# Performance work log

Measured on AMD Instinct MI355X. Metric: run time of the kernel, lower is better.

The kernel has to match this reference:

```python
import jax, jax.numpy as jnp
import numpy as np

V, B, NP, NJ = 5, 32, 20, 17
NB = 16
ND = 128
POSE_MIN_DEPTH, POSE_MAX_DEPTH = 2000.0, 8000.0
POSE_SIGMA = 100.0
KS = 11
HIDDEN_ROUGH, HIDDEN = 1024, 1024
BONES = np.array([[0,1],[0,2],[1,3],[2,4],[5,6],[5,7],[7,9],[6,8],[8,10],[5,11],[6,12],[11,12],[11,13],[13,15],[12,14],[14,16]], dtype=np.int32)


def setup_inputs() -> dict:
    key = jax.random.key(0)
    ks = jax.random.split(key, 12)
    wh = jnp.array([1920.0, 1080.0], jnp.float32)
    kpts = jax.random.uniform(ks[0], (V, B, NP, NJ, 2), jnp.float32) * wh
    pose_vis = jnp.ones((V, B, NP), jnp.float32)
    joint_vis = (jax.random.uniform(ks[1], (V, B, NP, NJ)) > 0.15).astype(jnp.float32)
    gt_pose_depths = jax.random.uniform(ks[2], (B, NP), jnp.float32, 2000.0, 8000.0)
    gt_joint_depths = jax.random.uniform(ks[3], (B, NP, NJ), jnp.float32, -100.0, 100.0)
    angles = np.linspace(-0.3, 0.3, V)
    Rs = np.stack([np.array([[np.cos(a), 0.0, np.sin(a)], [0.0, 1.0, 0.0], [-np.sin(a), 0.0, np.cos(a)]], dtype=np.float32) for a in angles])
    cam_R = jnp.broadcast_to(jnp.asarray(Rs)[:, None], (V, B, 3, 3))
    tvec = np.zeros((V, 3), np.float32); tvec[:, 0] = np.linspace(-500.0, 500.0, V)
    cam_T = jnp.broadcast_to(jnp.asarray(tvec)[:, None], (V, B, 3))
    cam_f = jnp.full((V, B, 2), 1400.0, jnp.float32)
    cam_c = jnp.broadcast_to(jnp.array([960.0, 540.0], jnp.float32), (V, B, 2))
    image_wh = jnp.broadcast_to(jnp.array([1920.0, 1080.0], jnp.float32), (V, B, 2))
    num_persons = jax.random.randint(ks[4], (V, B), 10, NP + 1, jnp.int32)
    Wr1 = jax.random.normal(ks[5], (HIDDEN_ROUGH, NJ * 2)) * 0.02
    br1 = jnp.zeros((HIDDEN_ROUGH,), jnp.float32)
    Wr2 = jax.random.normal(ks[6], (NJ, HIDDEN_ROUGH)) * 0.02
    br2 = jnp.zeros((NJ,), jnp.float32)
    Wc1 = jax.random.normal(ks[7], (HIDDEN, NJ + NB, 3)) * 0.02
    bc1 = jnp.zeros((HIDDEN,), jnp.float32)
    Wc2 = jax.random.normal(ks[8], (1, HIDDEN, 3)) * 0.02
    bc2 = jnp.zeros((1,), jnp.float32)
    bones = jnp.asarray(BONES)
    return dict(kpts=kpts, pose_vis=pose_vis, joint_vis=joint_vis, gt_pose_depths=gt_pose_depths, gt_joint_depths=gt_joint_depths, cam_R=cam_R, cam_T=cam_T, cam_f=cam_f, cam_c=cam_c, image_wh=image_wh, num_persons=num_persons, Wr1=Wr1, br1=br1, Wr2=Wr2, br2=br2, Wc1=Wc1, bc1=bc1, Wc2=Wc2, bc2=bc2, bones=bones)


def _bone_len(p, bones):
    # p: [B, Np, Nj, D, 2] -> [B, Np, Nb, D]
    a = p[:, :, bones[:, 0]]
    b = p[:, :, bones[:, 1]]
    return jnp.sqrt(jnp.sum((a - b) ** 2, -1) + 1e-12)


def _conv1d(x, w, b):
    # x [N,C,L], w [O,I,3]
    y = jax.lax.conv_general_dilated(x, w, (1,), 'SAME', dimension_numbers=('NCH', 'OIH', 'NCH'))
    return y + b[None, :, None]


def _forward(kpts, joint_vis, cam_R, cam_T, cam_f, cam_c, image_wh, num_persons, Wr1, br1, Wr2, br2, Wc1, bc1, Wc2, bc2, bones):
    V_, B_, NP_, NJ_, _ = kpts.shape
    labels = jnp.arange(ND, dtype=jnp.float32) / (ND - 1) * (POSE_MAX_DEPTH - POSE_MIN_DEPTH) + POSE_MIN_DEPTH
    kt = kpts[0]  # target-view 2D poses [B,Np,Nj,2]
    # faithful to original indexing quirk: normalize all batches by batch-0 image size
    kn = kt / image_wh[0, 0][None, None, None, :]
    x = kn.reshape(B_ * NP_, NJ_ * 2)
    h = jax.nn.relu(x @ Wr1.T + br1)
    rough = (h @ Wr2.T + br2).reshape(B_, NP_, NJ_) * 1000.0
    rough = jax.lax.stop_gradient(rough)  # .detach() in original
    depths = labels[None, None, None, :] + rough[..., None]  # [B,Np,Nj,D]
    # back-project target 2D poses at every depth hypothesis
    R0, T0, f0, c0 = cam_R[0], cam_T[0], cam_f[0], cam_c[0]
    uvn = (kt - c0[:, None, None, :]) / f0[:, None, None, :]
    xy = uvn[..., None, :] * depths[..., None]
    cam_pts = jnp.concatenate([xy, depths[..., None]], -1)
    p3d = jnp.einsum('bji,bpkdj->bpkdi', R0, cam_pts) + T0[:, None, None, None, :]  # world [B,Np,Nj,D,3]

    scores = scores2 = boundings = boundings2 = None
    for rv in range(1, V_):
        Rr, Tr, fr, cr = cam_R[rv], cam_T[rv], cam_f[rv], cam_c[rv]
        xc = jnp.einsum('bij,bpkdj->bpkdi', Rr, p3d - Tr[:, None, None, None, :])
        p2t = xc[..., :2] / (xc[..., 2:3] + 1e-8) * fr[:, None, None, None, :] + cr[:, None, None, None, :]
        pr = kpts[rv]         # [B,Npr,Nj,2]
        vr = joint_vis[rv]    # [B,Npr,Nj]
        # pairwise dist over (target-person, ref-person) per joint/depth
        d = jnp.sum((p2t[:, :, None] - pr[:, None, :, :, None, :]) ** 2, -1)  # [B,Npt,Npr,Nj,D]
        w = vr[:, None, :, :, None]
        pdist = jnp.sum(d * w, 3) / (jnp.sum(w, 3) + 1e-8)  # [B,Npt,Npr,D]
        valid = jnp.arange(NP_)[None, None, :, None] < num_persons[rv][:, None, None, None]
        pdist = jnp.where(valid, pdist, 1e5)
        mm = jnp.argmin(pdist, 2)  # [B,Npt,D] nearest ref pose
        bidx = jnp.arange(B_)[:, None, None]
        matched = jnp.transpose(pr[bidx, mm], (0, 1, 3, 2, 4))  # [B,Npt,Nj,D,2]
        mvis = jnp.transpose(vr[bidx, mm], (0, 1, 3, 2))        # [B,Npt,Nj,D]
        mdist = jnp.sum((p2t - matched) ** 2, -1)
        score = jnp.exp(-jnp.sqrt(mdist + 1e-12) / POSE_SIGMA)  # panoptic branch
        score_bl = jnp.exp(-jnp.abs(_bone_len(matched, bones) - _bone_len(p2t, bones)) / 5.0)
        wimg = image_wh[rv][:, None, None, None, 0]
        himg = image_wh[rv][:, None, None, None, 1]
        inb = ((p2t[..., 0] >= 0) & (p2t[..., 1] >= 0) & (p2t[..., 0] <= wimg - 1) & (p2t[..., 1] <= himg - 1)).astype(score.dtype)
        bounding = inb * mvis
        bounding2 = jnp.broadcast_to(mvis[:, :, :1, :], score_bl.shape)
        if scores is None:
            scores, scores2 = score * bounding, score_bl * bounding2
            boundings, boundings2 = bounding, bounding2
        else:
            scores = scores + score * bounding
            scores2 = scores2 + score_bl * bounding2
            boundings = boundings + bounding
            boundings2 = boundings2 + bounding2
    psv = (scores / (boundings + 1e-8)).reshape(B_ * NP_, NJ_, ND)
    psv2 = (scores2 / (boundings2 + 1e-8)).reshape(B_ * NP_, NB, ND)
    xin = jnp.concatenate([psv, psv2], 1)  # [BN, Nj+Nb, D]
    hc = jax.nn.relu(_conv1d(xin, Wc1, bc1))
    logits = _conv1d(hc, Wc2, bc2)[:, 0, :]  # [BN, D]
    vol = jax.nn.softmax(logits, -1)
    # soft-argmax restricted to a window around the argmax
    pos = jnp.arange(ND, dtype=vol.dtype)
    idx = jnp.argmax(vol, -1)
    mask = (jnp.abs(pos[None, :] - idx[:, None].astype(vol.dtype)) <= KS // 2).astype(vol.dtype)
    mv = vol * mask
    mv = mv / (jnp.sum(mv, -1, keepdims=True) + 1e-8)
    pred_idx = jnp.sum(mv * pos, -1).reshape(B_, NP_)
    return pred_idx / (ND - 1) * (POSE_MAX_DEPTH - POSE_MIN_DEPTH) + POSE_MIN_DEPTH


def reference(kpts, pose_vis, joint_vis, gt_pose_depths, gt_joint_depths, cam_R, cam_T, cam_f, cam_c, image_wh, num_persons, Wr1, br1, Wr2, br2, Wc1, bc1, Wc2, bc2, bones):
    return _forward(kpts, joint_vis, cam_R, cam_T, cam_f, cam_c, image_wh, num_persons, Wr1, br1, Wr2, br2, Wc1, bc1, Wc2, bc2, bones)
```

## Files before the change

kernel.cpp:

```cpp
#include <hip/hip_runtime.h>
#include <math.h>

#define VV  5
#define BB  32
#define NPP 20
#define NJJ 17
#define NBB 16
#define NDD 128
#define HID 1024
#define KPITCH 128
#define KSTEPS 7
#define PRP 36
#define VRP 20
#define NCH 34
#define A_T_ELEMS (32 * KSTEPS * 64 * 8)
#define EPI_ELEMS (32 * 4 * 64 * 16)

typedef __attribute__((ext_vector_type(8))) short short8;
typedef __attribute__((ext_vector_type(16))) float float16;

static constexpr int BONE_A[NBB] = {0,0,1,2,5,5,7,6,8,5,6,11,11,13,12,14};
static constexpr int BONE_B[NBB] = {1,2,3,4,6,7,9,8,10,11,12,12,13,15,14,16};

__device__ __forceinline__ float warp_red_sum(float v) {
#pragma unroll
  for (int off = 32; off >= 1; off >>= 1) v += __shfl_xor(v, off, 64);
  return v;
}

__global__ __launch_bounds__(256) void prep_kernel(
    const float* __restrict__ Wc1, const float* __restrict__ Wc2,
    const float* __restrict__ bc1,
    unsigned short* __restrict__ A_hi, unsigned short* __restrict__ A_lo,
    float* __restrict__ epi) {
  int gidx = blockIdx.x * 256 + threadIdx.x;
  if (gidx < A_T_ELEMS) {
    int e = gidx & 7;
    int l = (gidx >> 3) & 63;
    int rest = gidx >> 9;
    int ks = rest % 7;
    int ot = rest / 7;
    int o = ot * 32 + (l & 31);
    int kk = ks * 16 + (l >> 5) * 8 + e;
    float x = (kk < 99) ? Wc1[o * 99 + kk] : 0.0f;
    unsigned int u = __float_as_uint(x);
    unsigned short hi = (unsigned short)(u >> 16);
    float xh = __uint_as_float((u >> 16) << 16);
    unsigned short lo = (unsigned short)(__float_as_uint(x - xh) >> 16);
    A_hi[gidx] = hi;
    A_lo[gidx] = lo;
  } else {
    int idx2 = gidx - A_T_ELEMS;
    if (idx2 < EPI_ELEMS) {
      int c = idx2 & 15;
      int l = (idx2 >> 4) & 63;
      int rb = (idx2 >> 10) & 3;
      int ot = idx2 >> 12;
      int base = ot * 32 + 4 * (l >> 5) + 8 * rb;
      epi[idx2] = (c < 12) ? Wc2[base * 3 + c] : bc1[base + (c - 12)];
    }
  }
}

__global__ __launch_bounds__(512, 4) void pose_front_kernel(
    const float* __restrict__ kpts, const float* __restrict__ joint_vis,
    const float* __restrict__ cam_R, const float* __restrict__ cam_T,
    const float* __restrict__ cam_f, const float* __restrict__ cam_c,
    const float* __restrict__ image_wh, const int* __restrict__ num_persons,
    const float* __restrict__ Wr1, const float* __restrict__ br1,
    const float* __restrict__ Wr2, const float* __restrict__ br2,
    float* __restrict__ ws_partial, float* __restrict__ ws_xin) {
  const int n = blockIdx.x;
  const int b = n / NPP;
  const int p = n % NPP;
  const int tid = threadIdx.x;
  const int wv = tid >> 6, ln = tid & 63;
  const int rvv = tid >> 7;
  const int d   = tid & (NDD - 1);

  __shared__ float sh_x[NJJ * 2];
  __shared__ float sh_h[HID];
  __shared__ float sh_rough[NJJ];
  __shared__ float sh_base[NJJ][3];
  __shared__ __align__(16) float sh_pr[4][NPP][PRP];
  __shared__ __align__(16) float sh_vr[4][NPP][VRP];

  if (tid < NJJ * 2) {
    int j = tid >> 1, c = tid & 1;
    float k = kpts[((size_t)(b * NPP + p)) * NJJ * 2 + j * 2 + c];
    sh_x[tid] = k / image_wh[c];
  }
  __syncthreads();

#pragma unroll
  for (int k = 0; k < 2; ++k) {
    int m = tid + k * 512;
    float acc = br1[m];
#pragma unroll
    for (int c = 0; c < NJJ * 2; ++c) acc = fmaf(Wr1[m * (NJJ * 2) + c], sh_x[c], acc);
    sh_h[m] = fmaxf(acc, 0.0f);
  }
  __syncthreads();

  for (int j = wv; j < NJJ; j += 8) {
    float part = 0.0f;
    for (int m = ln; m < HID; m += 64) part = fmaf(Wr2[j * HID + m], sh_h[m], part);
    part = warp_red_sum(part);
    if (ln == 0) sh_rough[j] = (part + br2[j]) * 1000.0f;
  }
  if (tid < NJJ) {
    int j = tid;
    const float* R0 = cam_R + (size_t)b * 9;
    float c0x = cam_c[b * 2 + 0], c0y = cam_c[b * 2 + 1];
    float f0x = cam_f[b * 2 + 0], f0y = cam_f[b * 2 + 1];
    float kx = kpts[((size_t)(b * NPP + p)) * NJJ * 2 + j * 2 + 0];
    float ky = kpts[((size_t)(b * NPP + p)) * NJJ * 2 + j * 2 + 1];
    float ux = (kx - c0x) / f0x;
    float uy = (ky - c0y) / f0y;
#pragma unroll
    for (int i = 0; i < 3; ++i)
      sh_base[j][i] = R0[0 * 3 + i] * ux + R0[1 * 3 + i] * uy + R0[2 * 3 + i];
  }
#pragma unroll
  for (int rr = 0; rr < 4; ++rr) {
    const float* prg = kpts + ((size_t)(rr + 1) * BB + b) * NPP * NJJ * 2;
    for (int idx = tid; idx < NPP * NJJ * 2; idx += 512)
      sh_pr[rr][idx / 34][idx % 34] = prg[idx];
    const float* vrg = joint_vis + ((size_t)(rr + 1) * BB + b) * NPP * NJJ;
    for (int idx = tid; idx < NPP * NJJ; idx += 512)
      sh_vr[rr][idx / 17][idx % 17] = vrg[idx];
  }
  if (tid < 4 * BB) {
    int rr = tid >> 5, q = tid & 31;
    if (q < NPP) {
      sh_pr[rr][q][34] = 0.0f; sh_pr[rr][q][35] = 0.0f;
      sh_vr[rr][q][17] = 0.0f; sh_vr[rr][q][18] = 0.0f; sh_vr[rr][q][19] = 0.0f;
    }
  }
  __syncthreads();

  {
    const int rv = rvv + 1;
    const int vb = rv * BB + b;
    const float* Rr = cam_R + (size_t)vb * 9;
    const float R00 = Rr[0], R01 = Rr[1], R02 = Rr[2];
    const float R10 = Rr[3], R11 = Rr[4], R12 = Rr[5];
    const float R20 = Rr[6], R21 = Rr[7], R22 = Rr[8];
    const float Trx = cam_T[vb * 3 + 0], Try = cam_T[vb * 3 + 1], Trz = cam_T[vb * 3 + 2];
    const float frx = cam_f[vb * 2 + 0], fry = cam_f[vb * 2 + 1];
    const float crx = cam_c[vb * 2 + 0], cry = cam_c[vb * 2 + 1];
    const float wmax = image_wh[vb * 2 + 0] - 1.0f;
    const float hmax = image_wh[vb * 2 + 1] - 1.0f;
    const int nprv = num_persons[vb];
    const float T0x = cam_T[b * 3 + 0], T0y = cam_T[b * 3 + 1], T0z = cam_T[b * 3 + 2];
    const float lab = ((float)d / 127.0f) * 6000.0f + 2000.0f;

    float px[NJJ], py[NJJ];
#pragma unroll
    for (int j = 0; j < NJJ; ++j) {
      float dep = lab + sh_rough[j];
      float p0 = fmaf(dep, sh_base[j][0], T0x);
      float p1 = fmaf(dep, sh_base[j][1], T0y);
      float p2 = fmaf(dep, sh_base[j][2], T0z);
      float q0 = p0 - Trx, q1 = p1 - Try, q2 = p2 - Trz;
      float xc0 = R00 * q0 + R01 * q1 + R02 * q2;
      float xc1 = R10 * q0 + R11 * q1 + R12 * q2;
      float xc2 = R20 * q0 + R21 * q1 + R22 * q2 + 1e-8f;
      px[j] = xc0 / xc2 * frx + crx;
      py[j] = xc1 / xc2 * fry + cry;
    }

    float best = 3.4e38f;
    int mm = 0;
#pragma unroll 1
    for (int q = 0; q < NPP; ++q) {
      const float4* pr4 = (const float4*)(&sh_pr[rvv][q][0]);
      const float4* vr4 = (const float4*)(&sh_vr[rvv][q][0]);
      float num = 0.0f, den = 0.0f;
#pragma unroll
      for (int g4 = 0; g4 < 4; ++g4) {
        float4 w  = vr4[g4];
        float4 pa = pr4[2 * g4 + 0];
        float4 pb = pr4[2 * g4 + 1];
        { float dx = px[4*g4+0] - pa.x, dy = py[4*g4+0] - pa.y; num = fmaf(w.x, dx*dx + dy*dy, num); den += w.x; }
        { float dx = px[4*g4+1] - pa.z, dy = py[4*g4+1] - pa.w; num = fmaf(w.y, dx*dx + dy*dy, num); den += w.y; }
        { float dx = px[4*g4+2] - pb.x, dy = py[4*g4+2] - pb.y; num = fmaf(w.z, dx*dx + dy*dy, num); den += w.z; }
        { float dx = px[4*g4+3] - pb.z, dy = py[4*g4+3] - pb.w; num = fmaf(w.w, dx*dx + dy*dy, num); den += w.w; }
      }
      {
        float w16 = sh_vr[rvv][q][16];
        float4 pc = pr4[8];
        float dx = px[16] - pc.x, dy = py[16] - pc.y;
        num = fmaf(w16, dx*dx + dy*dy, num); den += w16;
      }
      float pd = num / (den + 1e-8f);
      if (q >= nprv) pd = 100000.0f;
      if (pd < best) { best = pd; mm = q; }
    }

    float* pbase = ws_partial + (((size_t)n * NCH) * 4 + rvv) * 128 + d;
    unsigned int maskB = 0u;
#pragma unroll
    for (int j = 0; j < NJJ; ++j) {
      float mx = sh_pr[rvv][mm][j * 2 + 0];
      float my = sh_pr[rvv][mm][j * 2 + 1];
      float mv = sh_vr[rvv][mm][j];
      float dx = px[j] - mx, dy = py[j] - my;
      float sc = expf(-sqrtf(dx * dx + dy * dy + 1e-12f) / 100.0f);
      float inb = (px[j] >= 0.0f && py[j] >= 0.0f && px[j] <= wmax && py[j] <= hmax) ? 1.0f : 0.0f;
      float bd = inb * mv;
      pbase[j * 512] = sc * bd;
      maskB |= ((unsigned int)(bd != 0.0f)) << j;
    }
    float v0 = sh_vr[rvv][mm][0];
    maskB |= ((unsigned int)(v0 != 0.0f)) << 17;
#pragma unroll
    for (int nb = 0; nb < NBB; ++nb) {
      const int a = BONE_A[nb], c = BONE_B[nb];
      float ax = sh_pr[rvv][mm][a * 2 + 0], ay = sh_pr[rvv][mm][a * 2 + 1];
      float cx = sh_pr[rvv][mm][c * 2 + 0], cy = sh_pr[rvv][mm][c * 2 + 1];
      float dmx = ax - cx, dmy = ay - cy;
      float blm = sqrtf(dmx * dmx + dmy * dmy + 1e-12f);
      float dpx = px[a] - px[c], dpy = py[a] - py[c];
      float blp = sqrtf(dpx * dpx + dpy * dpy + 1e-12f);
      float scb = expf(-fabsf(blm - blp) / 5.0f);
      pbase[(NJJ + nb) * 512] = scb * v0;
    }
    *(unsigned int*)(pbase + 33 * 512) = maskB;
  }

  __syncthreads();
  {
    const float* pb = ws_partial + ((size_t)n * NCH) * 4 * 128;
    float* xo = ws_xin + (size_t)n * (NJJ + NBB) * NDD;
    const int t = tid & 127;
    unsigned int m0 = __float_as_uint(pb[(33 * 4 + 0) * 128 + t]);
    unsigned int m1 = __float_as_uint(pb[(33 * 4 + 1) * 128 + t]);
    unsigned int m2 = __float_as_uint(pb[(33 * 4 + 2) * 128 + t]);
    unsigned int m3 = __float_as_uint(pb[(33 * 4 + 3) * 128 + t]);
#pragma unroll 1
    for (int i = tid >> 7; i < NJJ + NBB; i += 4) {
      const float* a = pb + ((size_t)i * 4) * 128 + t;
      float s = ((a[0] + a[128]) + a[256]) + a[384];
      const int bit = (i < NJJ) ? i : 17;
      int cnt = ((m0 >> bit) & 1) + ((m1 >> bit) & 1) + ((m2 >> bit) & 1) + ((m3 >> bit) & 1);
      xo[i * NDD + t] = s / ((float)cnt + 1e-8f);
    }
  }
}

__global__ __launch_bounds__(512, 2) void conv_mfma_kernel(
    const float* __restrict__ ws_xin,
    const unsigned short* __restrict__ A_hi, const unsigned short* __restrict__ A_lo,
    const float* __restrict__ epi,
    const float* __restrict__ bc2, float* __restrict__ out) {
  const int n = blockIdx.x;
  const int tid = threadIdx.x;
  const int w = tid >> 6;
  const int l = tid & 63;
  const int lrow = l & 31;
  const int g = l >> 5;

  __shared__ __align__(16) unsigned short bT_hi[128 * KPITCH];
  __shared__ __align__(16) unsigned short bT_lo[128 * KPITCH];
  __shared__ float plg[3][8][NDD];
  __shared__ float sh_l[NDD];
  __shared__ float sh_e[NDD];
  __shared__ float sh_sc[2];

  for (int i = tid; i < 3 * 8 * NDD; i += 512) ((float*)plg)[i] = 0.0f;

  const float* xn = ws_xin + (size_t)n * (NJJ + NBB) * NDD;
  for (int idx = tid; idx < 64 * 128; idx += 512) {
    const int kp = (idx & 63) << 1;
    const int t  = idx >> 6;
    unsigned int hp = 0, lp = 0;
#pragma unroll
    for (int u = 0; u < 2; ++u) {
      const int kk = kp + u;
      float x = 0.0f;
      if (kk < 99) {
        int i3 = kk / 3;
        int k3 = kk - i3 * 3;
        int tt = t + k3 - 1;
        if (tt >= 0 && tt < 128) x = xn[i3 * NDD + tt];
      }
      unsigned int uu = __float_as_uint(x);
      unsigned int hi = uu >> 16;
      float xh = __uint_as_float(hi << 16);
      unsigned int lo = __float_as_uint(x - xh) >> 16;
      hp |= hi << (16 * u);
      lp |= lo << (16 * u);
    }
    const int e = t * KPITCH + (kp ^ ((t & 15) << 3));
    *(unsigned int*)(bT_hi + e) = hp;
    *(unsigned int*)(bT_lo + e) = lp;
  }
  __syncthreads();

#pragma unroll 1
  for (int otile = 0; otile < 4; ++otile) {
    const int otg = w * 4 + otile;

    short8 Ah[KSTEPS], Al[KSTEPS];
    {
      const short8* ahT = ((const short8*)A_hi) + (size_t)otg * KSTEPS * 64 + l;
      const short8* alT = ((const short8*)A_lo) + (size_t)otg * KSTEPS * 64 + l;
#pragma unroll
      for (int ks = 0; ks < KSTEPS; ++ks) {
        Ah[ks] = ahT[ks * 64];
        Al[ks] = alT[ks * 64];
      }
    }
    float w2f[48];
    float bcf[16];
#pragma unroll
    for (int rb = 0; rb < 4; ++rb) {
      const float4* ep = ((const float4*)epi) + ((size_t)(otg * 4 + rb) * 64 + l) * 4;
      float4 e0 = ep[0], e1 = ep[1], e2 = ep[2], e3 = ep[3];
      w2f[rb * 12 + 0] = e0.x;  w2f[rb * 12 + 1] = e0.y;  w2f[rb * 12 + 2] = e0.z;
      w2f[rb * 12 + 3] = e0.w;  w2f[rb * 12 + 4] = e1.x;  w2f[rb * 12 + 5] = e1.y;
      w2f[rb * 12 + 6] = e1.z;  w2f[rb * 12 + 7] = e1.w;  w2f[rb * 12 + 8] = e2.x;
      w2f[rb * 12 + 9] = e2.y;  w2f[rb * 12 + 10] = e2.z; w2f[rb * 12 + 11] = e2.w;
      bcf[rb * 4 + 0] = e3.x; bcf[rb * 4 + 1] = e3.y;
      bcf[rb * 4 + 2] = e3.z; bcf[rb * 4 + 3] = e3.w;
    }

#pragma unroll 1
    for (int ttile = 0; ttile < 4; ++ttile) {
      const int trow = ttile * 32 + lrow;
      const unsigned short* brh = bT_hi + trow * KPITCH;
      const unsigned short* brl = bT_lo + trow * KPITCH;
      const int sw = (trow & 15) << 3;

      float16 X, Y;
#pragma unroll
      for (int r = 0; r < 16; ++r) { X[r] = 0.0f; Y[r] = 0.0f; }

#pragma unroll
      for (int ks = 0; ks < KSTEPS; ++ks) {
        const int e = (ks * 16 + g * 8) ^ sw;
        short8 bh8 = *(const short8*)(brh + e);
        X = __builtin_amdgcn_mfma_f32_32x32x16_bf16(Ah[ks], bh8, X, 0, 0, 0);
        Y = __builtin_amdgcn_mfma_f32_32x32x16_bf16(Al[ks], bh8, Y, 0, 0, 0);
      }
#pragma unroll
      for (int ks = 0; ks < KSTEPS; ++ks) {
        const int e = (ks * 16 + g * 8) ^ sw;
        short8 bl8 = *(const short8*)(brl + e);
        if (ks & 1) Y = __builtin_amdgcn_mfma_f32_32x32x16_bf16(Ah[ks], bl8, Y, 0, 0, 0);
        else        X = __builtin_amdgcn_mfma_f32_32x32x16_bf16(Ah[ks], bl8, X, 0, 0, 0);
      }

      float sP = 0.0f, sC = 0.0f, sM = 0.0f;
#pragma unroll
      for (int r = 0; r < 16; ++r) {
        float h = fmaxf((X[r] + Y[r]) + bcf[(r >> 2) * 4 + (r & 3)], 0.0f);
        sP = fmaf(h, w2f[(r >> 2) * 12 + (r & 3) * 3 + 0], sP);
        sC = fmaf(h, w2f[(r >> 2) * 12 + (r & 3) * 3 + 1], sC);
        sM = fmaf(h, w2f[(r >> 2) * 12 + (r & 3) * 3 + 2], sM);
      }
      sP += __shfl_xor(sP, 32, 64);
      sC += __shfl_xor(sC, 32, 64);
      sM += __shfl_xor(sM, 32, 64);
      if (l < 32) {
        plg[0][w][trow] += sP;
        plg[1][w][trow] += sC;
        plg[2][w][trow] += sM;
      }
    }
  }
  __syncthreads();

  if (tid < NDD) {
    int t = tid;
    float lg = bc2[0];
#pragma unroll
    for (int ww = 0; ww < 8; ++ww) lg += plg[1][ww][t];
    if (t > 0) {
#pragma unroll
      for (int ww = 0; ww < 8; ++ww) lg += plg[0][ww][t - 1];
    }
    if (t < NDD - 1) {
#pragma unroll
      for (int ww = 0; ww < 8; ++ww) lg += plg[2][ww][t + 1];
    }
    sh_l[t] = lg;
  }
  __syncthreads();
  if (tid < 64) {
    float v1 = sh_l[tid], v2 = sh_l[tid + 64];
    float mv; int mi;
    if (v2 > v1) { mv = v2; mi = tid + 64; } else { mv = v1; mi = tid; }
#pragma unroll
    for (int off = 32; off >= 1; off >>= 1) {
      float ov = __shfl_xor(mv, off, 64);
      int   oi = __shfl_xor(mi, off, 64);
      if (ov > mv || (ov == mv && oi < mi)) { mv = ov; mi = oi; }
    }
    if (tid == 0) { sh_sc[0] = mv; ((int*)sh_sc)[1] = mi; }
  }
  __syncthreads();
  const float gmax = sh_sc[0];
  const int gidx = ((const int*)sh_sc)[1];
  if (tid < NDD) sh_e[tid] = expf(sh_l[tid] - gmax);
  __syncthreads();
  if (tid < 64) {
    float S = warp_red_sum(sh_e[tid] + sh_e[tid + 64]);
    float a1 = 0.0f, a2 = 0.0f;
#pragma unroll
    for (int k = 0; k < 2; ++k) {
      int t = tid + k * 64;
      float vol = sh_e[t] / S;
      float msk = (fabsf((float)t - (float)gidx) <= 5.0f) ? 1.0f : 0.0f;
      float mvv = vol * msk;
      a1 += mvv;
      a2 += mvv * (float)t;
    }
    a1 = warp_red_sum(a1);
    a2 = warp_red_sum(a2);
    if (tid == 0) {
      float pred = a2 / (a1 + 1e-8f);
      out[n] = pred / 127.0f * 6000.0f + 2000.0f;
    }
  }
}

extern "C" void kernel_launch(void* const* d_in, const int* in_sizes, int n_in,
                              void* d_out, int out_size, void* d_ws, size_t ws_size,
                              hipStream_t stream) {
  (void)in_sizes; (void)n_in; (void)out_size; (void)ws_size;
  const float* kpts        = (const float*)d_in[0];
  const float* joint_vis   = (const float*)d_in[2];
  const float* cam_R       = (const float*)d_in[5];
  const float* cam_T       = (const float*)d_in[6];
  const float* cam_f       = (const float*)d_in[7];
  const float* cam_c       = (const float*)d_in[8];
  const float* image_wh    = (const float*)d_in[9];
  const int*   num_persons = (const int*)d_in[10];
  const float* Wr1 = (const float*)d_in[11];
  const float* br1 = (const float*)d_in[12];
  const float* Wr2 = (const float*)d_in[13];
  const float* br2 = (const float*)d_in[14];
  const float* Wc1 = (const float*)d_in[15];
  const float* bc1 = (const float*)d_in[16];
  const float* Wc2 = (const float*)d_in[17];
  const float* bc2 = (const float*)d_in[18];
  float* out = (float*)d_out;

  unsigned short* A_hi = (unsigned short*)d_ws;
  unsigned short* A_lo = A_hi + A_T_ELEMS;
  float* epi        = (float*)(A_lo + A_T_ELEMS);
  float* ws_xin     = epi + EPI_ELEMS;
  float* ws_partial = ws_xin + (size_t)BB * NPP * (NJJ + NBB) * NDD;

  const int prep_items = A_T_ELEMS + EPI_ELEMS;
  hipLaunchKernelGGL(prep_kernel, dim3((prep_items + 255) / 256), dim3(256), 0, stream,
                     Wc1, Wc2, bc1, A_hi, A_lo, epi);
  hipLaunchKernelGGL(pose_front_kernel, dim3(BB * NPP), dim3(512), 0, stream,
                     kpts, joint_vis, cam_R, cam_T, cam_f, cam_c, image_wh,
                     num_persons, Wr1, br1, Wr2, br2, ws_partial, ws_xin);
  hipLaunchKernelGGL(conv_mfma_kernel, dim3(BB * NPP), dim3(512), 0, stream,
                     ws_xin, A_hi, A_lo, epi, bc2, out);
}
```

Measured before the change: 183.6 us.

## Fuse pose front kernel and conv MFMA kernel into one launch with shared-memory union

```diff
diff --git a/kernel.cpp b/kernel.cpp
--- a/kernel.cpp
+++ b/kernel.cpp
@@ -62,14 +62,36 @@
   }
 }
 
-__global__ __launch_bounds__(512, 4) void pose_front_kernel(
+union __align__(16) SMem {
+  struct {
+    float pr[4][NPP][PRP];
+    float vr[4][NPP][VRP];
+    float x[NJJ * 2];
+    float h[HID];
+    float rough[NJJ];
+    float base[NJJ][3];
+  } f;
+  struct {
+    unsigned short bt_hi[128 * KPITCH];
+    unsigned short bt_lo[128 * KPITCH];
+    float plg[3][8][NDD];
+    float l[NDD];
+    float e[NDD];
+    float sc[2];
+  } c;
+};
+
+__global__ __launch_bounds__(512, 2) void fused_kernel(
     const float* __restrict__ kpts, const float* __restrict__ joint_vis,
     const float* __restrict__ cam_R, const float* __restrict__ cam_T,
     const float* __restrict__ cam_f, const float* __restrict__ cam_c,
     const float* __restrict__ image_wh, const int* __restrict__ num_persons,
     const float* __restrict__ Wr1, const float* __restrict__ br1,
     const float* __restrict__ Wr2, const float* __restrict__ br2,
-    float* __restrict__ ws_partial, float* __restrict__ ws_xin) {
+    const unsigned short* __restrict__ A_hi, const unsigned short* __restrict__ A_lo,
+    const float* __restrict__ epi, const float* __restrict__ bc2,
+    float* __restrict__ ws_partial, float* __restrict__ ws_xin,
+    float* __restrict__ out) {
   const int n = blockIdx.x;
   const int b = n / NPP;
   const int p = n % NPP;
@@ -78,17 +100,12 @@
   const int rvv = tid >> 7;
   const int d   = tid & (NDD - 1);
 
-  __shared__ float sh_x[NJJ * 2];
-  __shared__ float sh_h[HID];
-  __shared__ float sh_rough[NJJ];
-  __shared__ float sh_base[NJJ][3];
-  __shared__ __align__(16) float sh_pr[4][NPP][PRP];
-  __shared__ __align__(16) float sh_vr[4][NPP][VRP];
+  __shared__ SMem sm;
 
   if (tid < NJJ * 2) {
     int j = tid >> 1, c = tid & 1;
     float k = kpts[((size_t)(b * NPP + p)) * NJJ * 2 + j * 2 + c];
-    sh_x[tid] = k / image_wh[c];
+    sm.f.x[tid] = k / image_wh[c];
   }
   __syncthreads();
 
@@ -97,16 +114,16 @@
     int m = tid + k * 512;
     float acc = br1[m];
 #pragma unroll
-    for (int c = 0; c < NJJ * 2; ++c) acc = fmaf(Wr1[m * (NJJ * 2) + c], sh_x[c], acc);
-    sh_h[m] = fmaxf(acc, 0.0f);
+    for (int c = 0; c < NJJ * 2; ++c) acc = fmaf(Wr1[m * (NJJ * 2) + c], sm.f.x[c], acc);
+    sm.f.h[m] = fmaxf(acc, 0.0f);
   }
   __syncthreads();
 
   for (int j = wv; j < NJJ; j += 8) {
     float part = 0.0f;
-    for (int m = ln; m < HID; m += 64) part = fmaf(Wr2[j * HID + m], sh_h[m], part);
+    for (int m = ln; m < HID; m += 64) part = fmaf(Wr2[j * HID + m], sm.f.h[m], part);
     part = warp_red_sum(part);
-    if (ln == 0) sh_rough[j] = (part + br2[j]) * 1000.0f;
+    if (ln == 0) sm.f.rough[j] = (part + br2[j]) * 1000.0f;
   }
   if (tid < NJJ) {
     int j = tid;
@@ -119,22 +136,22 @@
     float uy = (ky - c0y) / f0y;
 #pragma unroll
     for (int i = 0; i < 3; ++i)
-      sh_base[j][i] = R0[0 * 3 + i] * ux + R0[1 * 3 + i] * uy + R0[2 * 3 + i];
+      sm.f.base[j][i] = R0[0 * 3 + i] * ux + R0[1 * 3 + i] * uy + R0[2 * 3 + i];
   }
 #pragma unroll
   for (int rr = 0; rr < 4; ++rr) {
     const float* prg = kpts + ((size_t)(rr + 1) * BB + b) * NPP * NJJ * 2;
     for (int idx = tid; idx < NPP * NJJ * 2; idx += 512)
-      sh_pr[rr][idx / 34][idx % 34] = prg[idx];
+      sm.f.pr[rr][idx / 34][idx % 34] = prg[idx];
     const float* vrg = joint_vis + ((size_t)(rr + 1) * BB + b) * NPP * NJJ;
     for (int idx = tid; idx < NPP * NJJ; idx += 512)
-      sh_vr[rr][idx / 17][idx % 17] = vrg[idx];
+      sm.f.vr[rr][idx / 17][idx % 17] = vrg[idx];
   }
   if (tid < 4 * BB) {
     int rr = tid >> 5, q = tid & 31;
     if (q < NPP) {
-      sh_pr[rr][q][34] = 0.0f; sh_pr[rr][q][35] = 0.0f;
-      sh_vr[rr][q][17] = 0.0f; sh_vr[rr][q][18] = 0.0f; sh_vr[rr][q][19] = 0.0f;
+      sm.f.pr[rr][q][34] = 0.0f; sm.f.pr[rr][q][35] = 0.0f;
+      sm.f.vr[rr][q][17] = 0.0f; sm.f.vr[rr][q][18] = 0.0f; sm.f.vr[rr][q][19] = 0.0f;
     }
   }
   __syncthreads();
@@ -158,10 +175,10 @@
     float px[NJJ], py[NJJ];
 #pragma unroll
     for (int j = 0; j < NJJ; ++j) {
-      float dep = lab + sh_rough[j];
-      float p0 = fmaf(dep, sh_base[j][0], T0x);
-      float p1 = fmaf(dep, sh_base[j][1], T0y);
-      float p2 = fmaf(dep, sh_base[j][2], T0z);
+      float dep = lab + sm.f.rough[j];
+      float p0 = fmaf(dep, sm.f.base[j][0], T0x);
+      float p1 = fmaf(dep, sm.f.base[j][1], T0y);
+      float p2 = fmaf(dep, sm.f.base[j][2], T0z);
       float q0 = p0 - Trx, q1 = p1 - Try, q2 = p2 - Trz;
       float xc0 = R00 * q0 + R01 * q1 + R02 * q2;
       float xc1 = R10 * q0 + R11 * q1 + R12 * q2;
@@ -174,8 +191,8 @@
     int mm = 0;
 #pragma unroll 1
     for (int q = 0; q < NPP; ++q) {
-      const float4* pr4 = (const float4*)(&sh_pr[rvv][q][0]);
-      const float4* vr4 = (const float4*)(&sh_vr[rvv][q][0]);
+      const float4* pr4 = (const float4*)(&sm.f.pr[rvv][q][0]);
+      const float4* vr4 = (const float4*)(&sm.f.vr[rvv][q][0]);
       float num = 0.0f, den = 0.0f;
 #pragma unroll
       for (int g4 = 0; g4 < 4; ++g4) {
@@ -188,7 +205,7 @@
         { float dx = px[4*g4+3] - pb.z, dy = py[4*g4+3] - pb.w; num = fmaf(w.w, dx*dx + dy*dy, num); den += w.w; }
       }
       {
-        float w16 = sh_vr[rvv][q][16];
+        float w16 = sm.f.vr[rvv][q][16];
         float4 pc = pr4[8];
         float dx = px[16] - pc.x, dy = py[16] - pc.y;
         num = fmaf(w16, dx*dx + dy*dy, num); den += w16;
@@ -202,9 +219,9 @@
     unsigned int maskB = 0u;
 #pragma unroll
     for (int j = 0; j < NJJ; ++j) {
-      float mx = sh_pr[rvv][mm][j * 2 + 0];
-      float my = sh_pr[rvv][mm][j * 2 + 1];
-      float mv = sh_vr[rvv][mm][j];
+      float mx = sm.f.pr[rvv][mm][j * 2 + 0];
+      float my = sm.f.pr[rvv][mm][j * 2 + 1];
+      float mv = sm.f.vr[rvv][mm][j];
       float dx = px[j] - mx, dy = py[j] - my;
       float sc = expf(-sqrtf(dx * dx + dy * dy + 1e-12f) / 100.0f);
       float inb = (px[j] >= 0.0f && py[j] >= 0.0f && px[j] <= wmax && py[j] <= hmax) ? 1.0f : 0.0f;
@@ -212,13 +229,13 @@
       pbase[j * 512] = sc * bd;
       maskB |= ((unsigned int)(bd != 0.0f)) << j;
     }
-    float v0 = sh_vr[rvv][mm][0];
+    float v0 = sm.f.vr[rvv][mm][0];
     maskB |= ((unsigned int)(v0 != 0.0f)) << 17;
 #pragma unroll
     for (int nb = 0; nb < NBB; ++nb) {
       const int a = BONE_A[nb], c = BONE_B[nb];
-      float ax = sh_pr[rvv][mm][a * 2 + 0], ay = sh_pr[rvv][mm][a * 2 + 1];
-      float cx = sh_pr[rvv][mm][c * 2 + 0], cy = sh_pr[rvv][mm][c * 2 + 1];
+      float ax = sm.f.pr[rvv][mm][a * 2 + 0], ay = sm.f.pr[rvv][mm][a * 2 + 1];
+      float cx = sm.f.pr[rvv][mm][c * 2 + 0], cy = sm.f.pr[rvv][mm][c * 2 + 1];
       float dmx = ax - cx, dmy = ay - cy;
       float blm = sqrtf(dmx * dmx + dmy * dmy + 1e-12f);
       float dpx = px[a] - px[c], dpy = py[a] - py[c];
@@ -247,28 +264,14 @@
       xo[i * NDD + t] = s / ((float)cnt + 1e-8f);
     }
   }
-}
-
-__global__ __launch_bounds__(512, 2) void conv_mfma_kernel(
-    const float* __restrict__ ws_xin,
-    const unsigned short* __restrict__ A_hi, const unsigned short* __restrict__ A_lo,
-    const float* __restrict__ epi,
-    const float* __restrict__ bc2, float* __restrict__ out) {
-  const int n = blockIdx.x;
-  const int tid = threadIdx.x;
+  __syncthreads();
+
   const int w = tid >> 6;
   const int l = tid & 63;
   const int lrow = l & 31;
   const int g = l >> 5;
 
-  __shared__ __align__(16) unsigned short bT_hi[128 * KPITCH];
-  __shared__ __align__(16) unsigned short bT_lo[128 * KPITCH];
-  __shared__ float plg[3][8][NDD];
-  __shared__ float sh_l[NDD];
-  __shared__ float sh_e[NDD];
-  __shared__ float sh_sc[2];
-
-  for (int i = tid; i < 3 * 8 * NDD; i += 512) ((float*)plg)[i] = 0.0f;
+  for (int i = tid; i < 3 * 8 * NDD; i += 512) ((float*)sm.c.plg)[i] = 0.0f;
 
   const float* xn = ws_xin + (size_t)n * (NJJ + NBB) * NDD;
   for (int idx = tid; idx < 64 * 128; idx += 512) {
@@ -293,8 +296,8 @@
       lp |= lo << (16 * u);
     }
     const int e = t * KPITCH + (kp ^ ((t & 15) << 3));
-    *(unsigned int*)(bT_hi + e) = hp;
-    *(unsigned int*)(bT_lo + e) = lp;
+    *(unsigned int*)(sm.c.bt_hi + e) = hp;
+    *(unsigned int*)(sm.c.bt_lo + e) = lp;
   }
   __syncthreads();
 
@@ -329,8 +332,8 @@
 #pragma unroll 1
     for (int ttile = 0; ttile < 4; ++ttile) {
       const int trow = ttile * 32 + lrow;
-      const unsigned short* brh = bT_hi + trow * KPITCH;
-      const unsigned short* brl = bT_lo + trow * KPITCH;
+      const unsigned short* brh = sm.c.bt_hi + trow * KPITCH;
+      const unsigned short* brl = sm.c.bt_lo + trow * KPITCH;
       const int sw = (trow & 15) << 3;
 
       float16 X, Y;
@@ -364,9 +367,9 @@
       sC += __shfl_xor(sC, 32, 64);
       sM += __shfl_xor(sM, 32, 64);
       if (l < 32) {
-        plg[0][w][trow] += sP;
-        plg[1][w][trow] += sC;
-        plg[2][w][trow] += sM;
+        sm.c.plg[0][w][trow] += sP;
+        sm.c.plg[1][w][trow] += sC;
+        sm.c.plg[2][w][trow] += sM;
       }
     }
   }
@@ -376,20 +379,20 @@
     int t = tid;
     float lg = bc2[0];
 #pragma unroll
-    for (int ww = 0; ww < 8; ++ww) lg += plg[1][ww][t];
+    for (int ww = 0; ww < 8; ++ww) lg += sm.c.plg[1][ww][t];
     if (t > 0) {
 #pragma unroll
-      for (int ww = 0; ww < 8; ++ww) lg += plg[0][ww][t - 1];
+      for (int ww = 0; ww < 8; ++ww) lg += sm.c.plg[0][ww][t - 1];
     }
     if (t < NDD - 1) {
 #pragma unroll
-      for (int ww = 0; ww < 8; ++ww) lg += plg[2][ww][t + 1];
-    }
-    sh_l[t] = lg;
+      for (int ww = 0; ww < 8; ++ww) lg += sm.c.plg[2][ww][t + 1];
+    }
+    sm.c.l[t] = lg;
   }
   __syncthreads();
   if (tid < 64) {
-    float v1 = sh_l[tid], v2 = sh_l[tid + 64];
+    float v1 = sm.c.l[tid], v2 = sm.c.l[tid + 64];
     float mv; int mi;
     if (v2 > v1) { mv = v2; mi = tid + 64; } else { mv = v1; mi = tid; }
 #pragma unroll
@@ -398,20 +401,20 @@
       int   oi = __shfl_xor(mi, off, 64);
       if (ov > mv || (ov == mv && oi < mi)) { mv = ov; mi = oi; }
     }
-    if (tid == 0) { sh_sc[0] = mv; ((int*)sh_sc)[1] = mi; }
-  }
-  __syncthreads();
-  const float gmax = sh_sc[0];
-  const int gidx = ((const int*)sh_sc)[1];
-  if (tid < NDD) sh_e[tid] = expf(sh_l[tid] - gmax);
+    if (tid == 0) { sm.c.sc[0] = mv; ((int*)sm.c.sc)[1] = mi; }
+  }
+  __syncthreads();
+  const float gmax = sm.c.sc[0];
+  const int gidx = ((const int*)sm.c.sc)[1];
+  if (tid < NDD) sm.c.e[tid] = expf(sm.c.l[tid] - gmax);
   __syncthreads();
   if (tid < 64) {
-    float S = warp_red_sum(sh_e[tid] + sh_e[tid + 64]);
+    float S = warp_red_sum(sm.c.e[tid] + sm.c.e[tid + 64]);
     float a1 = 0.0f, a2 = 0.0f;
 #pragma unroll
     for (int k = 0; k < 2; ++k) {
       int t = tid + k * 64;
-      float vol = sh_e[t] / S;
+      float vol = sm.c.e[t] / S;
       float msk = (fabsf((float)t - (float)gidx) <= 5.0f) ? 1.0f : 0.0f;
       float mvv = vol * msk;
       a1 += mvv;
@@ -457,9 +460,8 @@
   const int prep_items = A_T_ELEMS + EPI_ELEMS;
   hipLaunchKernelGGL(prep_kernel, dim3((prep_items + 255) / 256), dim3(256), 0, stream,
                      Wc1, Wc2, bc1, A_hi, A_lo, epi);
-  hipLaunchKernelGGL(pose_front_kernel, dim3(BB * NPP), dim3(512), 0, stream,
+  hipLaunchKernelGGL(fused_kernel, dim3(BB * NPP), dim3(512), 0, stream,
                      kpts, joint_vis, cam_R, cam_T, cam_f, cam_c, image_wh,
-                     num_persons, Wr1, br1, Wr2, br2, ws_partial, ws_xin);
-  hipLaunchKernelGGL(conv_mfma_kernel, dim3(BB * NPP), dim3(512), 0, stream,
-                     ws_xin, A_hi, A_lo, epi, bc2, out);
+                     num_persons, Wr1, br1, Wr2, br2,
+                     A_hi, A_lo, epi, bc2, ws_partial, ws_xin, out);
 }
```

Result: slower. 205.9 us (+12.1%).
